# Optimization experiments

Hardware: AMD Instinct MI355X
Metric: run time of the kernel (lower is better)

## Reference

```python
import jax, jax.numpy as jnp
import numpy as np

EPS = 1e-7

# ---- Poincare ball (c=1) manifold ops ----

def _logmap0(y):
    n = jnp.linalg.norm(y, axis=-1, keepdims=True)
    n = jnp.clip(n, EPS, 1.0 - 1e-5)
    return jnp.arctanh(n) * y / n


def _expmap0(v):
    n = jnp.maximum(jnp.linalg.norm(v, axis=-1, keepdims=True), EPS)
    return jnp.tanh(n) * v / n


def _pair_dist(q):
    # q: [B,N,H,D] points in the Poincare ball.
    # d(x,y) = arccosh(1 + 2||x-y||^2 / ((1-||x||^2)(1-||y||^2)))  (== 2 artanh ||(-x)+_m y||)
    sq = jnp.sum(q * q, axis=-1)                       # [B,N,H]
    dot = jnp.einsum('bnhd,bmhd->bnmh', q, q)          # [B,N,N,H] (batched GEMM)
    diff = jnp.maximum(sq[:, :, None, :] + sq[:, None, :, :] - 2.0 * dot, 0.0)
    denom = jnp.maximum((1.0 - sq[:, :, None, :]) * (1.0 - sq[:, None, :, :]), EPS)
    return jnp.arccosh(jnp.maximum(1.0 + 2.0 * diff / denom, 1.0 + EPS))  # [B,N,N,H]


def _hgat(x, adj, W, a_src, a_dst, multihead):
    # Hyperbolic GAT layer: log-map to tangent at origin, per-head linear +
    # masked GAT attention, exp-map back. use_act=False, no bias.
    xt = _logmap0(x)                                   # [B,N,Din]
    h = jnp.einsum('bnd,hde->bnhe', xt, W)             # [B,N,H,D]
    es = jnp.einsum('bnhe,he->bnh', h, a_src)
    ed = jnp.einsum('bnhe,he->bnh', h, a_dst)
    e = jax.nn.leaky_relu(es[:, :, None, :] + ed[:, None, :, :], 0.2)  # [B,N,N,H]
    e = jnp.where(adj[:, :, :, None] > 0, e, -1e9)
    att = jax.nn.softmax(e, axis=2)                    # over neighbors
    out = jnp.einsum('bnmh,bmhe->bnhe', att, h)        # [B,N,H,D]
    if multihead:
        return _expmap0(out)                           # per-head hyperbolic points
    B, N, H, D = out.shape
    return _expmap0(out.reshape(B, N, H * D))          # concat heads


def setup_inputs() -> dict:
    key = jax.random.key(0)
    B, N, DIN, DATT, DOUT, H = 8, 1024, 256, 64, 256, 4
    ks = jax.random.split(key, 8)
    x = _expmap0(0.5 * jax.random.normal(ks[0], (B, N, DIN), dtype=jnp.float32))
    a0 = (jax.random.uniform(ks[1], (B, N, N)) < 0.05).astype(jnp.float32)
    adj = jnp.maximum(a0, jnp.swapaxes(a0, -1, -2))
    adj = jnp.maximum(adj, jnp.eye(N, dtype=jnp.float32)[None])
    flags = jnp.ones((B, N), dtype=jnp.float32)
    s_in = 1.0 / np.sqrt(DIN)
    Wq = jax.random.normal(ks[2], (H, DIN, DATT), dtype=jnp.float32) * s_in
    aq_src = jax.random.normal(ks[3], (H, DATT), dtype=jnp.float32) / np.sqrt(DATT)
    aq_dst = jax.random.normal(ks[4], (H, DATT), dtype=jnp.float32) / np.sqrt(DATT)
    Dv = DOUT // H
    Wv = jax.random.normal(ks[5], (H, DIN, Dv), dtype=jnp.float32) * s_in
    av_src = jax.random.normal(ks[6], (H, Dv), dtype=jnp.float32) / np.sqrt(Dv)
    av_dst = jax.random.normal(ks[7], (H, Dv), dtype=jnp.float32) / np.sqrt(Dv)
    r = jnp.ones((H,), dtype=jnp.float32) * 5.0
    t = jnp.ones((H,), dtype=jnp.float32)
    return {"x": x, "adj": adj, "flags": flags, "Wq": Wq, "aq_src": aq_src,
            "aq_dst": aq_dst, "Wv": Wv, "av_src": av_src, "av_dst": av_dst,
            "r": r, "t": t}


def reference(x, adj, flags, Wq, aq_src, aq_dst, Wv, av_src, av_dst, r, t):
    B, N = adj.shape[0], adj.shape[1]
    query = _hgat(x, adj, Wq, aq_src, aq_dst, True)    # [B,N,H,DATT]
    value = _hgat(x, adj, Wv, av_src, av_dst, False)   # [B,N,DOUT]
    dist = _pair_dist(query)                           # [B,N,N,H]
    dist = dist.reshape(-1, B, N, N)                   # faithful torch .view(-1,*adj.shape)
    att = jnp.tanh((r[:, None, None, None] - dist) * t[:, None, None, None])
    att = att.reshape(-1, B, N, N).mean(axis=0)        # head-average -> [B,N,N]
    att = (att + jnp.swapaxes(att, -1, -2)) / 2.0      # symmetrize
    return value, att
```

## Files before the change

### kernel.cpp

```cpp
#include <hip/hip_runtime.h>
#include <hip/hip_bf16.h>
#include <math.h>

#define DEV __device__ __forceinline__

constexpr int B = 8, N = 1024, DIN = 256, H = 4, DATT = 64, DV = 64;
constexpr int BN = B * N;
constexpr int HD = H * DATT;
constexpr int HDV = H * DV;
constexpr int COLS = HD + HDV;
constexpr int BHN = B * H * N;
constexpr float EPSF = 1e-7f;

using short8 = __attribute__((ext_vector_type(8))) short;
using f32x4  = __attribute__((ext_vector_type(4))) float;

DEV unsigned short f2bf(float f) {
    __hip_bfloat16 h = __float2bfloat16(f);
    return *reinterpret_cast<unsigned short*>(&h);
}
DEV float bfu2f(unsigned short u) { return __uint_as_float(((unsigned)u) << 16); }

DEV void tsplit(float v, short& hs, short& ls) {
    unsigned vu = __float_as_uint(v);
    float lo = v - __uint_as_float(vu & 0xFFFF0000u);
    hs = (short)(unsigned short)(vu >> 16);
    ls = (short)(unsigned short)(__float_as_uint(lo) >> 16);
}

__global__ void k_scale(const float* __restrict__ x, float* __restrict__ s) {
    int p = blockIdx.x * 4 + (threadIdx.x >> 6);
    int l = threadIdx.x & 63;
    const float4* xr = reinterpret_cast<const float4*>(x + (size_t)p * DIN);
    float4 u = xr[l];
    float ss = u.x * u.x + u.y * u.y + u.z * u.z + u.w * u.w;
    for (int m = 32; m; m >>= 1) ss += __shfl_xor(ss, m);
    if (l == 0) {
        float n = sqrtf(ss);
        n = fminf(fmaxf(n, EPSF), 1.0f - 1e-5f);
        float at = 0.5f * __logf((1.f + n) / (1.f - n));
        s[p] = at / n;
    }
}

__global__ void k_wcat(const float* __restrict__ Wq, const float* __restrict__ Wv,
                       float* __restrict__ Wc) {
    int idx = blockIdx.x * 256 + threadIdx.x;
    int k = idx >> 9, c = idx & 511;
    int cc = c & 255;
    int h = cc >> 6, e = cc & 63;
    const float* src = (c < HD) ? Wq : Wv;
    Wc[idx] = src[(h * DIN + k) * 64 + e];
}

__global__ __launch_bounds__(256) void k_gemm(const float* __restrict__ x,
                                              const float* __restrict__ s,
                                              const float* __restrict__ Wc,
                                              float* __restrict__ hall) {
    __shared__ float As[16][68];
    __shared__ float Bs[16][68];
    int bm = blockIdx.x, bn = blockIdx.y;
    int tid = threadIdx.x;
    int ty = tid >> 4, tx = tid & 15;
    float acc[4][4] = {};
    int rowbase = bm * 64, colbase = bn * 64;
    int am = tid >> 2;
    int ak = (tid & 3) * 4;
    float sc = s[rowbase + am];
    for (int kt = 0; kt < DIN; kt += 16) {
        float4 u = *reinterpret_cast<const float4*>(x + (size_t)(rowbase + am) * DIN + kt + ak);
        As[ak + 0][am] = u.x * sc;
        As[ak + 1][am] = u.y * sc;
        As[ak + 2][am] = u.z * sc;
        As[ak + 3][am] = u.w * sc;
        int bk = tid >> 4, bc = (tid & 15) * 4;
        float4 w4 = *reinterpret_cast<const float4*>(Wc + (size_t)(kt + bk) * COLS + colbase + bc);
        *reinterpret_cast<float4*>(&Bs[bk][bc]) = w4;
        __syncthreads();
        for (int k = 0; k < 16; k++) {
            float4 a4 = *reinterpret_cast<const float4*>(&As[k][ty * 4]);
            float4 b4 = *reinterpret_cast<const float4*>(&Bs[k][tx * 4]);
            float av[4] = {a4.x, a4.y, a4.z, a4.w};
            float bv[4] = {b4.x, b4.y, b4.z, b4.w};
            for (int i = 0; i < 4; i++)
                for (int j = 0; j < 4; j++) acc[i][j] = fmaf(av[i], bv[j], acc[i][j]);
        }
        __syncthreads();
    }
    for (int i = 0; i < 4; i++) {
        float4 o = make_float4(acc[i][0], acc[i][1], acc[i][2], acc[i][3]);
        *reinterpret_cast<float4*>(hall + (size_t)(rowbase + ty * 4 + i) * COLS + colbase + tx * 4) = o;
    }
}

__global__ __launch_bounds__(256) void k_hT(const float* __restrict__ hall,
                                            unsigned short* __restrict__ hallT) {
    int jt = blockIdx.x, h = blockIdx.y, b = blockIdx.z;
    __shared__ float T[64][69];
    int t = threadIdx.x;
    int bh = b * H + h;
    int jl = t >> 2, cg = t & 3;
    int el = t >> 2, seg = t & 3;
    #pragma unroll
    for (int pass = 0; pass < 2; pass++) {
        int colbase = (pass == 0) ? h * 64 : 256 + h * 64;
        __syncthreads();
        {
            const float* src = hall + (size_t)(b * N + jt * 64 + jl) * COLS + colbase + cg * 16;
            #pragma unroll
            for (int u = 0; u < 4; u++) {
                float4 v = *reinterpret_cast<const float4*>(src + u * 4);
                T[jl][cg * 16 + u * 4 + 0] = v.x;
                T[jl][cg * 16 + u * 4 + 1] = v.y;
                T[jl][cg * 16 + u * 4 + 2] = v.z;
                T[jl][cg * 16 + u * 4 + 3] = v.w;
            }
        }
        __syncthreads();
        {
            unsigned int pk[8];
            #pragma unroll
            for (int k = 0; k < 8; k++) {
                float f0 = T[seg * 16 + 2 * k][el];
                float f1 = T[seg * 16 + 2 * k + 1][el];
                pk[k] = (unsigned)f2bf(f0) | ((unsigned)f2bf(f1) << 16);
            }
            unsigned short* dst = hallT + ((size_t)(bh * 128 + pass * 64 + el)) * 1024
                                  + jt * 64 + seg * 16;
            *reinterpret_cast<uint4*>(dst)     = make_uint4(pk[0], pk[1], pk[2], pk[3]);
            *reinterpret_cast<uint4*>(dst + 8) = make_uint4(pk[4], pk[5], pk[6], pk[7]);
        }
    }
}

__global__ void k_esed(const float* __restrict__ hall, const float* __restrict__ aqs,
                       const float* __restrict__ aqd, const float* __restrict__ avs,
                       const float* __restrict__ avd, float* __restrict__ esq,
                       float* __restrict__ edq, float* __restrict__ esv,
                       float* __restrict__ edv) {
    int p = blockIdx.x;
    int h = threadIdx.x >> 6, e = threadIdx.x & 63;
    float hq = hall[(size_t)p * COLS + h * 64 + e];
    float hv = hall[(size_t)p * COLS + 256 + h * 64 + e];
    float v1 = hq * aqs[h * 64 + e];
    float v2 = hq * aqd[h * 64 + e];
    float v3 = hv * avs[h * 64 + e];
    float v4 = hv * avd[h * 64 + e];
    for (int m = 32; m; m >>= 1) {
        v1 += __shfl_xor(v1, m); v2 += __shfl_xor(v2, m);
        v3 += __shfl_xor(v3, m); v4 += __shfl_xor(v4, m);
    }
    if (e == 0) {
        int b = p >> 10, n = p & 1023;
        int o = (b * H + h) * N + n;
        esq[o] = v1; edq[o] = v2; esv[o] = v3; edv[o] = v4;
    }
}

__global__ void k_stats(const float* __restrict__ adj, const float* __restrict__ esq,
                        const float* __restrict__ edq, const float* __restrict__ esv,
                        const float* __restrict__ edv, float* __restrict__ stats,
                        unsigned char* __restrict__ amask) {
    int bid = blockIdx.x;
    int i = bid & 1023;
    int bh = bid >> 10;
    int b = bh >> 2;
    int t = threadIdx.x;
    float esqi = esq[bid], esvi = esv[bid];
    const float* arow = adj + (size_t)(b * N + i) * N + t * 8;
    const float* edqr = edq + (size_t)bh * N + t * 8;
    const float* edvr = edv + (size_t)bh * N + t * 8;
    float4 a0 = *reinterpret_cast<const float4*>(arow);
    float4 a1 = *reinterpret_cast<const float4*>(arow + 4);
    float am[8] = {a0.x, a0.y, a0.z, a0.w, a1.x, a1.y, a1.z, a1.w};
    float4 q0 = *reinterpret_cast<const float4*>(edqr);
    float4 q1 = *reinterpret_cast<const float4*>(edqr + 4);
    float4 w0 = *reinterpret_cast<const float4*>(edvr);
    float4 w1 = *reinterpret_cast<const float4*>(edvr + 4);
    float edqv[8] = {q0.x, q0.y, q0.z, q0.w, q1.x, q1.y, q1.z, q1.w};
    float edvv[8] = {w0.x, w0.y, w0.z, w0.w, w1.x, w1.y, w1.z, w1.w};
    float eq[8], ev[8];
    unsigned mb = 0;
    float mq = -1e30f, mv = -1e30f;
    for (int j = 0; j < 8; j++) {
        bool msk = am[j] > 0.f;
        mb |= (unsigned)msk << j;
        float q = esqi + edqv[j]; q = fmaxf(q, 0.2f * q);
        float v = esvi + edvv[j]; v = fmaxf(v, 0.2f * v);
        eq[j] = msk ? q : -1e30f;
        ev[j] = msk ? v : -1e30f;
        mq = fmaxf(mq, eq[j]); mv = fmaxf(mv, ev[j]);
    }
    if ((bh & 3) == 0)
        amask[(size_t)(b * N + i) * 128 + t] = (unsigned char)mb;
    __shared__ float red[2][2];
    __shared__ float red2[2][2];
    for (int m = 32; m; m >>= 1) { mq = fmaxf(mq, __shfl_xor(mq, m)); mv = fmaxf(mv, __shfl_xor(mv, m)); }
    int w = t >> 6;
    if ((t & 63) == 0) { red[w][0] = mq; red[w][1] = mv; }
    __syncthreads();
    mq = fmaxf(red[0][0], red[1][0]);
    mv = fmaxf(red[0][1], red[1][1]);
    float sq_ = 0.f, sv_ = 0.f;
    for (int j = 0; j < 8; j++) { sq_ += __expf(eq[j] - mq); sv_ += __expf(ev[j] - mv); }
    for (int m = 32; m; m >>= 1) { sq_ += __shfl_xor(sq_, m); sv_ += __shfl_xor(sv_, m); }
    if ((t & 63) == 0) { red2[w][0] = sq_; red2[w][1] = sv_; }
    __syncthreads();
    if (t == 0) {
        stats[bid] = mq;
        stats[BHN + bid] = red2[0][0] + red2[1][0];
        stats[2 * BHN + bid] = mv;
        stats[3 * BHN + bid] = red2[0][1] + red2[1][1];
    }
}

__global__ __launch_bounds__(512) void k_aggr(const unsigned char* __restrict__ amask,
        const unsigned short* __restrict__ hallT, const float* __restrict__ esq,
        const float* __restrict__ edq, const float* __restrict__ esv,
        const float* __restrict__ edv, const float* __restrict__ stats,
        float* __restrict__ outq, float* __restrict__ outv) {
    int f = blockIdx.x;
    int g = ((f & 7) << 7) | (f >> 3);
    int b = g >> 7;
    int it = (g >> 2) & 31;
    int h = g & 3;
    int bh = b * H + h;
    int i0 = it * 32;
    int t = threadIdx.x;
    int lane = t & 63, wv = t >> 6;
    int team = wv >> 1;
    int mh = wv & 1;

    int i = i0 + mh * 16 + (lane & 15);
    int bi = bh * N + i;
    float esq_i = esq[bi], esv_i = esv[bi];
    float mq_i = stats[bi];           float isq_i = 1.f / stats[BHN + bi];
    float mv_i = stats[2 * BHN + bi]; float isv_i = 1.f / stats[3 * BHN + bi];
    const unsigned char* mrow = amask + (size_t)(b * N + i) * 128;
    const float* edqrow = edq + (size_t)bh * N;
    const float* edvrow = edv + (size_t)bh * N;
    int klo = lane >> 4;
    const unsigned short* bbq = hallT
        + ((size_t)(bh * 128 + (lane & 15))) * 1024 + klo * 8;
    const unsigned short* bbv = bbq + (size_t)64 * 1024;

    f32x4 accq[4] = {}, accv[4] = {};
    int jbase = team * 256;
    for (int jj = 0; jj < 8; jj++) {
        int j0 = jbase + jj * 32;
        unsigned mword = *reinterpret_cast<const unsigned*>(mrow + (j0 >> 3));
        float4 q0 = *reinterpret_cast<const float4*>(edqrow + j0 + klo * 8);
        float4 q1 = *reinterpret_cast<const float4*>(edqrow + j0 + klo * 8 + 4);
        float4 v0 = *reinterpret_cast<const float4*>(edvrow + j0 + klo * 8);
        float4 v1 = *reinterpret_cast<const float4*>(edvrow + j0 + klo * 8 + 4);
        float eq[8] = {q0.x, q0.y, q0.z, q0.w, q1.x, q1.y, q1.z, q1.w};
        float ev[8] = {v0.x, v0.y, v0.z, v0.w, v1.x, v1.y, v1.z, v1.w};
        short8 afq, afv;
        #pragma unroll
        for (int u = 0; u < 8; u++) {
            bool on = (mword >> (klo * 8 + u)) & 1;
            float q = esq_i + eq[u]; q = fmaxf(q, 0.2f * q);
            float v = esv_i + ev[u]; v = fmaxf(v, 0.2f * v);
            float wq = on ? __expf(q - mq_i) * isq_i : 0.f;
            float wvv = on ? __expf(v - mv_i) * isv_i : 0.f;
            afq[u] = (short)f2bf(wq);
            afv[u] = (short)f2bf(wvv);
        }
        #pragma unroll
        for (int nt = 0; nt < 4; nt++) {
            short8 bq = *reinterpret_cast<const short8*>(bbq + j0 + nt * 16384);
            accq[nt] = __builtin_amdgcn_mfma_f32_16x16x32_bf16(afq, bq, accq[nt], 0, 0, 0);
            short8 bv = *reinterpret_cast<const short8*>(bbv + j0 + nt * 16384);
            accv[nt] = __builtin_amdgcn_mfma_f32_16x16x32_bf16(afv, bv, accv[nt], 0, 0, 0);
        }
    }

    __shared__ __align__(16) float red[8192];
    int slot = (team >> 1) * 2 + mh;
    float* buf = red + slot * 2048;
    __syncthreads();
    if (team & 1) {
        #pragma unroll
        for (int k = 0; k < 4; k++) {
            *reinterpret_cast<f32x4*>(&buf[(k * 64 + lane) * 4])       = accq[k];
            *reinterpret_cast<f32x4*>(&buf[((k + 4) * 64 + lane) * 4]) = accv[k];
        }
    }
    __syncthreads();
    if (!(team & 1)) {
        #pragma unroll
        for (int k = 0; k < 4; k++) {
            f32x4 pq = *reinterpret_cast<const f32x4*>(&buf[(k * 64 + lane) * 4]);
            f32x4 pv = *reinterpret_cast<const f32x4*>(&buf[((k + 4) * 64 + lane) * 4]);
            accq[k] += pq; accv[k] += pv;
        }
    }
    __syncthreads();
    if (team == 2) {
        float* d2 = red + mh * 2048;
        #pragma unroll
        for (int k = 0; k < 4; k++) {
            *reinterpret_cast<f32x4*>(&d2[(k * 64 + lane) * 4])       = accq[k];
            *reinterpret_cast<f32x4*>(&d2[((k + 4) * 64 + lane) * 4]) = accv[k];
        }
    }
    __syncthreads();
    if (team == 0) {
        float* s2 = red + mh * 2048;
        #pragma unroll
        for (int nt = 0; nt < 4; nt++) {
            f32x4 pq = *reinterpret_cast<const f32x4*>(&s2[(nt * 64 + lane) * 4]);
            f32x4 pv = *reinterpret_cast<const f32x4*>(&s2[((nt + 4) * 64 + lane) * 4]);
            #pragma unroll
            for (int r = 0; r < 4; r++) {
                int irow = i0 + mh * 16 + (lane >> 4) * 4 + r;
                int e = nt * 16 + (lane & 15);
                outq[(size_t)(b * N + irow) * 256 + h * 64 + e] = accq[nt][r] + pq[r];
                outv[(size_t)(b * N + irow) * 256 + h * 64 + e] = accv[nt][r] + pv[r];
            }
        }
    }
}

__global__ void k_expmap(const float* __restrict__ outq, const float* __restrict__ outv,
                         unsigned short* __restrict__ qh, unsigned short* __restrict__ ql,
                         float* __restrict__ sq, float* __restrict__ isr,
                         float* __restrict__ val) {
    int p = blockIdx.x, t = threadIdx.x;
    int h = t >> 6, e = t & 63;
    float v = outq[(size_t)p * HD + t];
    float ss = v * v;
    for (int m = 32; m; m >>= 1) ss += __shfl_xor(ss, m);
    float n = fmaxf(sqrtf(ss), EPSF);
    float tn = tanhf(n);
    float qv = v * (tn / n);
    short hs, ls; tsplit(qv, hs, ls);
    qh[((size_t)p << 8) + t] = (unsigned short)hs;
    ql[((size_t)p << 8) + t] = (unsigned short)ls;
    if (e == 0) {
        float s = tn * tn;
        sq[h * BN + p] = s;
        isr[h * BN + p] = __builtin_amdgcn_rcpf(1.f - s);
    }

    float vv = outv[(size_t)p * HDV + t];
    float s2 = vv * vv;
    for (int m = 32; m; m >>= 1) s2 += __shfl_xor(s2, m);
    __shared__ float part[4];
    if (e == 0) part[h] = s2;
    __syncthreads();
    float tot = part[0] + part[1] + part[2] + part[3];
    float nv = fmaxf(sqrtf(tot), EPSF);
    float sclv = tanhf(nv) / nv;
    val[(size_t)p * HDV + t] = vv * sclv;
}

__global__ __launch_bounds__(256) void k_att(const unsigned short* __restrict__ qh,
        const unsigned short* __restrict__ ql, const float* __restrict__ sq,
        const float* __restrict__ isr, const float* __restrict__ rr,
        const float* __restrict__ tt, float* __restrict__ m_out) {
    int f = blockIdx.x;
    int g = ((f & 7) << 7) | (f >> 3);
    int b2 = g >> 7;
    int rem = g & 127;
    int c = rem >> 5, h = (rem >> 3) & 3, kc = (rem >> 1) & 3, xh = rem & 1;
    int t = threadIdx.x;
    int l = t & 63, w = t >> 6;
    int klo = l >> 4;

    int nstart = (b2 * 256 + kc * 64) & 1023;
    int mstart = c * 256 + xh * 128;

    float tacc[8][4] = {};

    #pragma unroll
    for (int a = 0; a < 4; a++) {
        int b = 2 * a + (b2 >> 2);
        size_t xbase = ((size_t)(b * N + nstart + w * 16 + (l & 15)) << 8) + h * 64 + klo * 8;
        short8 Ah[2], Al[2];
        #pragma unroll
        for (int kk = 0; kk < 2; kk++) {
            Ah[kk] = *reinterpret_cast<const short8*>(qh + xbase + kk * 32);
            Al[kk] = *reinterpret_cast<const short8*>(ql + xbase + kk * 32);
        }
        float ra = rr[a], ta = tt[a];
        float c1 = 2.f * ta;
        float c0 = c1 * ra * 1.44269504f;
        float sxr[4], ixr[4];
        #pragma unroll
        for (int r = 0; r < 4; r++) {
            int gx = h * BN + b * N + nstart + w * 16 + (l >> 4) * 4 + r;
            sxr[r] = sq[gx];
            ixr[r] = 2.f * isr[gx];
        }
        size_t ybase = ((size_t)(b * N + mstart + (l & 15)) << 8) + h * 64 + klo * 8;
        #pragma unroll
        for (int nt = 0; nt < 8; nt++) {
            size_t yb = ybase + ((size_t)(nt * 16) << 8);
            f32x4 acc = {};
            #pragma unroll
            for (int kk = 0; kk < 2; kk++) {
                short8 Bh = *reinterpret_cast<const short8*>(qh + yb + kk * 32);
                short8 Bl = *reinterpret_cast<const short8*>(ql + yb + kk * 32);
                acc = __builtin_amdgcn_mfma_f32_16x16x32_bf16(Ah[kk], Bh, acc, 0, 0, 0);
                acc = __builtin_amdgcn_mfma_f32_16x16x32_bf16(Ah[kk], Bl, acc, 0, 0, 0);
                acc = __builtin_amdgcn_mfma_f32_16x16x32_bf16(Al[kk], Bh, acc, 0, 0, 0);
            }
            int gy = h * BN + b * N + mstart + nt * 16 + (l & 15);
            float sy = sq[gy];
            float iy = isr[gy];
            #pragma unroll
            for (int r = 0; r < 4; r++) {
                float diff = fmaxf(fmaf(-2.f, acc[r], sxr[r] + sy), 0.f);
                float ixy = fminf(ixr[r] * iy, 2e7f);
                float z = fmaxf(fmaf(diff, ixy, 1.f), 1.f + EPSF);
                float s_ = z + __builtin_amdgcn_sqrtf(fmaf(z, z, -1.f));
                float l2 = __builtin_amdgcn_logf(s_);
                float ex = __builtin_amdgcn_exp2f(fmaf(-c1, l2, c0));
                float rc = __builtin_amdgcn_rcpf(ex + 1.f);
                tacc[nt][r] += fmaf(-2.f, rc, 1.f);
            }
        }
    }
    #pragma unroll
    for (int nt = 0; nt < 8; nt++) {
        #pragma unroll
        for (int r = 0; r < 4; r++) {
            int n_local = w * 16 + (l >> 4) * 4 + r;
            int n2 = c + 4 * (kc * 64 + n_local);
            int mloc = xh * 128 + nt * 16 + (l & 15);
            int m2 = 4 * mloc + h;
            m_out[((size_t)b2 << 20) + ((size_t)n2 << 10) + m2] = 0.25f * tacc[nt][r];
        }
    }
}

__global__ void k_sym(float* __restrict__ m) {
    int ti = blockIdx.x, tj = blockIdx.y, b = blockIdx.z;
    if (ti > tj) return;
    __shared__ float A[32][33], Bt[32][33];
    int t = threadIdx.x;
    int r = t >> 3, c4 = (t & 7) * 4;
    size_t baseA = ((size_t)b << 20) + (size_t)(ti * 32) * N + tj * 32;
    size_t baseB = ((size_t)b << 20) + (size_t)(tj * 32) * N + ti * 32;
    float4 ua = *reinterpret_cast<const float4*>(m + baseA + (size_t)r * N + c4);
    float4 ub = *reinterpret_cast<const float4*>(m + baseB + (size_t)r * N + c4);
    A[r][c4 + 0] = ua.x; A[r][c4 + 1] = ua.y; A[r][c4 + 2] = ua.z; A[r][c4 + 3] = ua.w;
    Bt[r][c4 + 0] = ub.x; Bt[r][c4 + 1] = ub.y; Bt[r][c4 + 2] = ub.z; Bt[r][c4 + 3] = ub.w;
    __syncthreads();
    for (int u = 0; u < 4; u++) {
        int cc = c4 + u;
        float oa = 0.5f * (A[r][cc] + Bt[cc][r]);
        float ob = 0.5f * (Bt[r][cc] + A[cc][r]);
        m[baseA + (size_t)r * N + cc] = oa;
        m[baseB + (size_t)r * N + cc] = ob;
    }
}

extern "C" void kernel_launch(void* const* d_in, const int* in_sizes, int n_in,
                              void* d_out, int out_size, void* d_ws, size_t ws_size,
                              hipStream_t stream) {
    const float* x   = (const float*)d_in[0];
    const float* adj = (const float*)d_in[1];
    const float* Wq  = (const float*)d_in[3];
    const float* aqs = (const float*)d_in[4];
    const float* aqd = (const float*)d_in[5];
    const float* Wv  = (const float*)d_in[6];
    const float* avs = (const float*)d_in[7];
    const float* avd = (const float*)d_in[8];
    const float* rr  = (const float*)d_in[9];
    const float* tt  = (const float*)d_in[10];

    float* ws = (float*)d_ws;
    float* s     = ws;
    float* Wc    = s + BN;
    float* hall  = Wc + 256 * COLS;
    float* esq   = hall + (size_t)BN * COLS;
    float* edq   = esq + BHN;
    float* esv   = edq + BHN;
    float* edv   = esv + BHN;
    float* stats = edv + BHN;
    float* outq  = stats + 4 * BHN;
    float* outv  = outq + (size_t)BN * HD;
    float* sq    = outv + (size_t)BN * HDV;
    unsigned short* hallT = (unsigned short*)(sq + H * BN);
    unsigned char* amask = (unsigned char*)(hallT + (size_t)BN * COLS);
    size_t need = (size_t)((char*)(amask + (size_t)BN * 128) - (char*)ws);
    if (ws_size < need) return;

    unsigned short* qh = (unsigned short*)hall;
    unsigned short* ql = qh + (size_t)BN * 256;
    float* isr = (float*)(ql + (size_t)BN * 256);

    float* val  = (float*)d_out;
    float* matt = (float*)d_out + (size_t)BN * HDV;

    k_scale<<<BN / 4, 256, 0, stream>>>(x, s);
    k_wcat<<<(256 * COLS) / 256, 256, 0, stream>>>(Wq, Wv, Wc);
    k_gemm<<<dim3(BN / 64, COLS / 64), 256, 0, stream>>>(x, s, Wc, hall);
    k_hT<<<dim3(16, H, B), 256, 0, stream>>>(hall, hallT);
    k_esed<<<BN, 256, 0, stream>>>(hall, aqs, aqd, avs, avd, esq, edq, esv, edv);
    k_stats<<<BHN, 128, 0, stream>>>(adj, esq, edq, esv, edv, stats, amask);
    k_aggr<<<1024, 512, 0, stream>>>(amask, hallT, esq, edq, esv, edv, stats, outq, outv);
    k_expmap<<<BN, 256, 0, stream>>>(outq, outv, qh, ql, sq, isr, val);
    k_att<<<1024, 256, 0, stream>>>(qh, ql, sq, isr, rr, tt, matt);
    k_sym<<<dim3(32, 32, 8), 256, 0, stream>>>(matt);
}
```

Before: 257.8 us.

## Fuse attention-logit dot products into transpose kernel and loop heads in stats

Computes the GAT source and destination logit projections inside the hall transpose kernel from the shared-memory tile, so the separate k_esed launch and its re-read of hall go away. The stats kernel now runs one block per (batch,row) and loops over the four heads. Each adjacency row is read and bit-packed once instead of four times. This cuts a launch and redundant adjacency traffic. In exchange each stats block works serially with extra barriers, and there are four times fewer blocks.

```diff
diff --git a/kernel.cpp b/kernel.cpp
--- a/kernel.cpp
+++ b/kernel.cpp
@@ -94,7 +94,10 @@
 }
 
 __global__ __launch_bounds__(256) void k_hT(const float* __restrict__ hall,
-                                            unsigned short* __restrict__ hallT) {
+        const float* __restrict__ aqs, const float* __restrict__ aqd,
+        const float* __restrict__ avs, const float* __restrict__ avd,
+        unsigned short* __restrict__ hallT, float* __restrict__ esq,
+        float* __restrict__ edq, float* __restrict__ esv, float* __restrict__ edv) {
     int jt = blockIdx.x, h = blockIdx.y, b = blockIdx.z;
     __shared__ float T[64][69];
     int t = threadIdx.x;
@@ -104,6 +107,10 @@
     #pragma unroll
     for (int pass = 0; pass < 2; pass++) {
         int colbase = (pass == 0) ? h * 64 : 256 + h * 64;
+        const float* as = (pass == 0) ? aqs : avs;
+        const float* ad = (pass == 0) ? aqd : avd;
+        float* es = (pass == 0) ? esq : esv;
+        float* ed = (pass == 0) ? edq : edv;
         __syncthreads();
         {
             const float* src = hall + (size_t)(b * N + jt * 64 + jl) * COLS + colbase + cg * 16;
@@ -130,30 +137,21 @@
             *reinterpret_cast<uint4*>(dst)     = make_uint4(pk[0], pk[1], pk[2], pk[3]);
             *reinterpret_cast<uint4*>(dst + 8) = make_uint4(pk[4], pk[5], pk[6], pk[7]);
         }
-    }
-}
-
-__global__ void k_esed(const float* __restrict__ hall, const float* __restrict__ aqs,
-                       const float* __restrict__ aqd, const float* __restrict__ avs,
-                       const float* __restrict__ avd, float* __restrict__ esq,
-                       float* __restrict__ edq, float* __restrict__ esv,
-                       float* __restrict__ edv) {
-    int p = blockIdx.x;
-    int h = threadIdx.x >> 6, e = threadIdx.x & 63;
-    float hq = hall[(size_t)p * COLS + h * 64 + e];
-    float hv = hall[(size_t)p * COLS + 256 + h * 64 + e];
-    float v1 = hq * aqs[h * 64 + e];
-    float v2 = hq * aqd[h * 64 + e];
-    float v3 = hv * avs[h * 64 + e];
-    float v4 = hv * avd[h * 64 + e];
-    for (int m = 32; m; m >>= 1) {
-        v1 += __shfl_xor(v1, m); v2 += __shfl_xor(v2, m);
-        v3 += __shfl_xor(v3, m); v4 += __shfl_xor(v4, m);
-    }
-    if (e == 0) {
-        int b = p >> 10, n = p & 1023;
-        int o = (b * H + h) * N + n;
-        esq[o] = v1; edq[o] = v2; esv[o] = v3; edv[o] = v4;
+        {
+            float p1 = 0.f, p2 = 0.f;
+            #pragma unroll
+            for (int u = 0; u < 16; u++) {
+                float hv = T[jl][cg * 16 + u];
+                p1 = fmaf(hv, as[h * 64 + cg * 16 + u], p1);
+                p2 = fmaf(hv, ad[h * 64 + cg * 16 + u], p2);
+            }
+            p1 += __shfl_xor(p1, 1); p2 += __shfl_xor(p2, 1);
+            p1 += __shfl_xor(p1, 2); p2 += __shfl_xor(p2, 2);
+            if (cg == 0) {
+                es[(size_t)bh * N + jt * 64 + jl] = p1;
+                ed[(size_t)bh * N + jt * 64 + jl] = p2;
+            }
+        }
     }
 }
 
@@ -161,56 +159,62 @@
                         const float* __restrict__ edq, const float* __restrict__ esv,
                         const float* __restrict__ edv, float* __restrict__ stats,
                         unsigned char* __restrict__ amask) {
-    int bid = blockIdx.x;
-    int i = bid & 1023;
-    int bh = bid >> 10;
-    int b = bh >> 2;
+    int pid = blockIdx.x;
+    int b = pid >> 10, i = pid & 1023;
     int t = threadIdx.x;
-    float esqi = esq[bid], esvi = esv[bid];
-    const float* arow = adj + (size_t)(b * N + i) * N + t * 8;
-    const float* edqr = edq + (size_t)bh * N + t * 8;
-    const float* edvr = edv + (size_t)bh * N + t * 8;
+    const float* arow = adj + (size_t)pid * N + t * 8;
     float4 a0 = *reinterpret_cast<const float4*>(arow);
     float4 a1 = *reinterpret_cast<const float4*>(arow + 4);
     float am[8] = {a0.x, a0.y, a0.z, a0.w, a1.x, a1.y, a1.z, a1.w};
-    float4 q0 = *reinterpret_cast<const float4*>(edqr);
-    float4 q1 = *reinterpret_cast<const float4*>(edqr + 4);
-    float4 w0 = *reinterpret_cast<const float4*>(edvr);
-    float4 w1 = *reinterpret_cast<const float4*>(edvr + 4);
-    float edqv[8] = {q0.x, q0.y, q0.z, q0.w, q1.x, q1.y, q1.z, q1.w};
-    float edvv[8] = {w0.x, w0.y, w0.z, w0.w, w1.x, w1.y, w1.z, w1.w};
-    float eq[8], ev[8];
     unsigned mb = 0;
-    float mq = -1e30f, mv = -1e30f;
-    for (int j = 0; j < 8; j++) {
-        bool msk = am[j] > 0.f;
-        mb |= (unsigned)msk << j;
-        float q = esqi + edqv[j]; q = fmaxf(q, 0.2f * q);
-        float v = esvi + edvv[j]; v = fmaxf(v, 0.2f * v);
-        eq[j] = msk ? q : -1e30f;
-        ev[j] = msk ? v : -1e30f;
-        mq = fmaxf(mq, eq[j]); mv = fmaxf(mv, ev[j]);
-    }
-    if ((bh & 3) == 0)
-        amask[(size_t)(b * N + i) * 128 + t] = (unsigned char)mb;
+    #pragma unroll
+    for (int j = 0; j < 8; j++) mb |= (unsigned)(am[j] > 0.f) << j;
+    amask[(size_t)pid * 128 + t] = (unsigned char)mb;
+
     __shared__ float red[2][2];
     __shared__ float red2[2][2];
-    for (int m = 32; m; m >>= 1) { mq = fmaxf(mq, __shfl_xor(mq, m)); mv = fmaxf(mv, __shfl_xor(mv, m)); }
     int w = t >> 6;
-    if ((t & 63) == 0) { red[w][0] = mq; red[w][1] = mv; }
-    __syncthreads();
-    mq = fmaxf(red[0][0], red[1][0]);
-    mv = fmaxf(red[0][1], red[1][1]);
-    float sq_ = 0.f, sv_ = 0.f;
-    for (int j = 0; j < 8; j++) { sq_ += __expf(eq[j] - mq); sv_ += __expf(ev[j] - mv); }
-    for (int m = 32; m; m >>= 1) { sq_ += __shfl_xor(sq_, m); sv_ += __shfl_xor(sv_, m); }
-    if ((t & 63) == 0) { red2[w][0] = sq_; red2[w][1] = sv_; }
-    __syncthreads();
-    if (t == 0) {
-        stats[bid] = mq;
-        stats[BHN + bid] = red2[0][0] + red2[1][0];
-        stats[2 * BHN + bid] = mv;
-        stats[3 * BHN + bid] = red2[0][1] + red2[1][1];
+    for (int h = 0; h < H; h++) {
+        int bh = b * H + h;
+        float esqi = esq[(size_t)bh * N + i], esvi = esv[(size_t)bh * N + i];
+        const float* edqr = edq + (size_t)bh * N + t * 8;
+        const float* edvr = edv + (size_t)bh * N + t * 8;
+        float4 q0 = *reinterpret_cast<const float4*>(edqr);
+        float4 q1 = *reinterpret_cast<const float4*>(edqr + 4);
+        float4 w0 = *reinterpret_cast<const float4*>(edvr);
+        float4 w1 = *reinterpret_cast<const float4*>(edvr + 4);
+        float edqv[8] = {q0.x, q0.y, q0.z, q0.w, q1.x, q1.y, q1.z, q1.w};
+        float edvv[8] = {w0.x, w0.y, w0.z, w0.w, w1.x, w1.y, w1.z, w1.w};
+        float eq[8], ev[8];
+        float mq = -1e30f, mv = -1e30f;
+        #pragma unroll
+        for (int j = 0; j < 8; j++) {
+            bool msk = (mb >> j) & 1;
+            float q = esqi + edqv[j]; q = fmaxf(q, 0.2f * q);
+            float v = esvi + edvv[j]; v = fmaxf(v, 0.2f * v);
+            eq[j] = msk ? q : -1e30f;
+            ev[j] = msk ? v : -1e30f;
+            mq = fmaxf(mq, eq[j]); mv = fmaxf(mv, ev[j]);
+        }
+        for (int m = 32; m; m >>= 1) { mq = fmaxf(mq, __shfl_xor(mq, m)); mv = fmaxf(mv, __shfl_xor(mv, m)); }
+        if ((t & 63) == 0) { red[w][0] = mq; red[w][1] = mv; }
+        __syncthreads();
+        mq = fmaxf(red[0][0], red[1][0]);
+        mv = fmaxf(red[0][1], red[1][1]);
+        float sq_ = 0.f, sv_ = 0.f;
+        #pragma unroll
+        for (int j = 0; j < 8; j++) { sq_ += __expf(eq[j] - mq); sv_ += __expf(ev[j] - mv); }
+        for (int m = 32; m; m >>= 1) { sq_ += __shfl_xor(sq_, m); sv_ += __shfl_xor(sv_, m); }
+        if ((t & 63) == 0) { red2[w][0] = sq_; red2[w][1] = sv_; }
+        __syncthreads();
+        if (t == 0) {
+            int bid = bh * N + i;
+            stats[bid] = mq;
+            stats[BHN + bid] = red2[0][0] + red2[1][0];
+            stats[2 * BHN + bid] = mv;
+            stats[3 * BHN + bid] = red2[0][1] + red2[1][1];
+        }
+        __syncthreads();
     }
 }
 
@@ -498,9 +502,9 @@
     k_scale<<<BN / 4, 256, 0, stream>>>(x, s);
     k_wcat<<<(256 * COLS) / 256, 256, 0, stream>>>(Wq, Wv, Wc);
     k_gemm<<<dim3(BN / 64, COLS / 64), 256, 0, stream>>>(x, s, Wc, hall);
-    k_hT<<<dim3(16, H, B), 256, 0, stream>>>(hall, hallT);
-    k_esed<<<BN, 256, 0, stream>>>(hall, aqs, aqd, avs, avd, esq, edq, esv, edv);
-    k_stats<<<BHN, 128, 0, stream>>>(adj, esq, edq, esv, edv, stats, amask);
+    k_hT<<<dim3(16, H, B), 256, 0, stream>>>(hall, aqs, aqd, avs, avd,
+                                             hallT, esq, edq, esv, edv);
+    k_stats<<<BN, 128, 0, stream>>>(adj, esq, edq, esv, edv, stats, amask);
     k_aggr<<<1024, 512, 0, stream>>>(amask, hallT, esq, edq, esv, edv, stats, outq, outv);
     k_expmap<<<BN, 256, 0, stream>>>(outq, outv, qh, ql, sq, isr, val);
     k_att<<<1024, 256, 0, stream>>>(qh, ql, sq, isr, rr, tt, matt);
```

Result: faster. 250.5 us (-2.8%).
